# Performance work log

Hardware: AMD Instinct MI355X
Metric: run time of the kernel (lower is better)

## Reference

```python
import jax, jax.numpy as jnp
import numpy as np

RADIUS = 0.12
N_SAMPLE = 32


def ball_query(radius, n_sample, xyz, new_xyz):
    """Faithful replication of pointnet2 ball_query CUDA semantics.

    For each query point, take the FIRST n_sample points (in index order)
    with squared distance < radius^2. If fewer than n_sample are found,
    remaining slots repeat the first found index. If none found, idx = 0.
    """
    B, N, _ = xyz.shape
    # d2[b,p,n] = ||new_xyz[b,p] - xyz[b,n]||^2 via expansion (avoids [B,P,N,3])
    qq = jnp.sum(new_xyz * new_xyz, axis=-1)[:, :, None]          # [B,P,1]
    xx = jnp.sum(xyz * xyz, axis=-1)[:, None, :]                  # [B,1,N]
    qx = jnp.einsum('bpd,bnd->bpn', new_xyz, xyz)                 # [B,P,N]
    d2 = qq + xx - 2.0 * qx
    mask = d2 < radius * radius
    # score = N - n for in-ball points (strictly decreasing in n), 0 otherwise.
    # top_k then yields the first n_sample in-ball indices in ascending n order.
    score = jnp.where(mask, (N - jnp.arange(N, dtype=jnp.int32))[None, None, :],
                      jnp.int32(0))
    vals, idx = jax.lax.top_k(score, n_sample)                    # [B,P,S]
    valid = vals > 0
    first = jnp.where(valid[..., :1], idx[..., :1], 0)            # 0 if no neighbor
    return jnp.where(valid, idx, first).astype(jnp.int32)


def group(features, idx):
    """features: [B,C,N], idx: [B,P,S] -> [B,C,P,S]."""
    return jax.vmap(lambda f, i: f[:, i])(features, idx)


def setup_inputs() -> dict:
    key = jax.random.key(0)
    k1, k2, k3 = jax.random.split(key, 3)
    B, N, P, C = 4, 8192, 2048, 64
    xyz = jax.random.uniform(k1, (B, N, 3), dtype=jnp.float32)
    new_xyz = jax.random.uniform(k2, (B, P, 3), dtype=jnp.float32)
    features = jax.random.normal(k3, (B, C, N), dtype=jnp.float32)
    return {"xyz": xyz, "new_xyz": new_xyz, "features": features}


def reference(xyz, new_xyz, features):
    idx = ball_query(RADIUS, N_SAMPLE, xyz, new_xyz)              # [B,P,S] int32
    xyz_t = jnp.transpose(xyz, (0, 2, 1))                         # [B,3,N]
    grouped_xyz = group(xyz_t, idx)                               # [B,3,P,S]
    grouped_xyz = grouped_xyz - jnp.transpose(new_xyz, (0, 2, 1))[..., None]
    grouped_features = group(features, idx)                       # [B,C,P,S]
    return jnp.concatenate([grouped_xyz, grouped_features], axis=1)  # [B,3+C,P,S]
```

## Files before the change

### kernel.cpp

```cpp
#include <hip/hip_runtime.h>

constexpr int kB = 4;
constexpr int kN = 8192;
constexpr int kP = 2048;
constexpr int kS = 32;
constexpr int kC = 64;
constexpr int kCO = 67;
constexpr float kR2 = 0.0144f;

__device__ __forceinline__ float sq3(float x, float y, float z) {
  return __fadd_rn(__fadd_rn(__fmul_rn(x, x), __fmul_rn(y, y)),
                   __fmul_rn(z, z));
}
__device__ __forceinline__ float dot3(float ax, float ay, float az, float bx,
                                      float by, float bz) {
  return __fadd_rn(__fadd_rn(__fmul_rn(ax, bx), __fmul_rn(ay, by)),
                   __fmul_rn(az, bz));
}

__global__ __launch_bounds__(256) void bq_k3(const float* __restrict__ xyz,
                                             const float* __restrict__ new_xyz,
                                             int* __restrict__ g_idx) {
  __shared__ unsigned short sidx[4][32];
  __shared__ int scnt[4];

  const int tid = threadIdx.x;
  const int wv = tid >> 6;
  const int lane = tid & 63;
  const int q = blockIdx.x * 4 + wv;
  const int b = q >> 11;
  const int p = q & (kP - 1);

  const float* xb = xyz + (size_t)b * kN * 3;
  const float* qb = new_xyz + ((size_t)b * kP + p) * 3;

  const float qx = qb[0], qy = qb[1], qz = qb[2];
  const float qq = sq3(qx, qy, qz);

  const unsigned long long lmask = (1ull << lane) - 1ull;
  int cnt = 0;

  float cx[4], cy[4], cz[4];
#pragma unroll
  for (int k = 0; k < 4; ++k) {
    int n = k * 64 + lane;
    cx[k] = xb[3 * n + 0];
    cy[k] = xb[3 * n + 1];
    cz[k] = xb[3 * n + 2];
  }

  int gbase = 0;
  for (int g0 = 256;; g0 += 256) {
    const bool more = (g0 < kN);
    const int g1 = more ? g0 : 0;
    float nx[4], ny[4], nz[4];
#pragma unroll
    for (int k = 0; k < 4; ++k) {
      int n = g1 + k * 64 + lane;
      nx[k] = xb[3 * n + 0];
      ny[k] = xb[3 * n + 1];
      nz[k] = xb[3 * n + 2];
    }
#pragma unroll
    for (int k = 0; k < 4; ++k) {
      const float px = cx[k], py = cy[k], pz = cz[k];
      const float xx = sq3(px, py, pz);
      const int ncur = gbase + k * 64 + lane;
      float d2 = __fsub_rn(__fadd_rn(qq, xx),
                           __fmul_rn(2.0f, dot3(qx, qy, qz, px, py, pz)));
      unsigned long long m = __ballot(d2 < kR2);
      if (m) {
        int pos = cnt + __popcll(m & lmask);
        if ((d2 < kR2) && pos < kS)
          sidx[wv][pos] = (unsigned short)ncur;
        cnt += __popcll(m);
      }
    }
    if (!more || cnt >= kS) break;
#pragma unroll
    for (int k = 0; k < 4; ++k) {
      cx[k] = nx[k];
      cy[k] = ny[k];
      cz[k] = nz[k];
    }
    gbase = g0;
  }

  if (lane == 0) scnt[wv] = cnt;
  __syncthreads();

  if (lane < kS) {
    int c = scnt[wv];
    int first = (c > 0) ? (int)sidx[wv][0] : 0;
    int val = (lane < c) ? (int)sidx[wv][lane] : first;
    g_idx[((size_t)(b * kP + p)) * kS + lane] = val;
  }
}

__global__ __launch_bounds__(512) void gather_k2(
    const float* __restrict__ xyz, const float* __restrict__ new_xyz,
    const float* __restrict__ feat, const int* __restrict__ g_idx,
    float* __restrict__ out) {
  __shared__ float row[kN];
  __shared__ float nxz[kP / 2];
  const int tid = threadIdx.x;
  const int bi = blockIdx.x;
  const int b = bi / (kCO * 2);
  const int r = bi % (kCO * 2);
  const int c = r >> 1;
  const int ph = r & 1;

  if (c < 3) {
    for (int i = tid; i < kN; i += 512)
      row[i] = xyz[((size_t)b * kN + i) * 3 + c];
    for (int i = tid; i < kP / 2; i += 512)
      nxz[i] = new_xyz[((size_t)b * kP + ph * (kP / 2) + i) * 3 + c];
  } else {
    const float4* src = (const float4*)(feat + ((size_t)b * kC + (c - 3)) * kN);
    float4* dst = (float4*)row;
    for (int i = tid; i < kN / 4; i += 512) dst[i] = src[i];
  }
  __syncthreads();

  const size_t eg_base = (((size_t)b * kP + ph * (kP / 2)) * kS) >> 2;
  const int4* idx4 = (const int4*)g_idx + eg_base;
  float4* out4 =
      (float4*)out + ((((size_t)b * kCO + c) * kP + ph * (kP / 2)) * kS >> 2);
  const bool isxyz = (c < 3);
#pragma unroll 4
  for (int it = 0; it < (kP / 2) * kS / 4 / 512; ++it) {
    const int e4 = it * 512 + tid;
    const int4 n = idx4[e4];
    float4 v = make_float4(row[n.x], row[n.y], row[n.z], row[n.w]);
    if (isxyz) {
      const float sub = nxz[e4 >> 3];
      v.x = __fsub_rn(v.x, sub);
      v.y = __fsub_rn(v.y, sub);
      v.z = __fsub_rn(v.z, sub);
      v.w = __fsub_rn(v.w, sub);
    }
    out4[e4] = v;
  }
}

__global__ __launch_bounds__(512) void fused_qg(
    const float* __restrict__ xyz, const float* __restrict__ new_xyz,
    const float* __restrict__ feat, float* __restrict__ out) {
  __shared__ __align__(16) char ls[32768 + 512 + 4096];
  unsigned short (*sidx)[64][32] = (unsigned short (*)[64][32])ls;
  float* row = (float*)ls;
  unsigned char (*scnt)[64] = (unsigned char (*)[64])(ls + 32768);
  unsigned short (*midx)[32] = (unsigned short (*)[32])(ls + 32768 + 512);

  const int tid = threadIdx.x;
  const int wv = tid >> 6;
  const int lane = tid & 63;
  const int b = blockIdx.x >> 5;
  const int p0 = (blockIdx.x & 31) << 6;

  {
    const float* q = &new_xyz[(b * kP + p0 + lane) * 3];
    const float qx = q[0], qy = q[1], qz = q[2];
    const float qq = sq3(qx, qy, qz);
    const float* xb = xyz + ((size_t)b * kN + wv * 1024) * 3;
    int cnt = 0;
    for (int i = 0; i < 1024; ++i) {
      float px = xb[i * 3 + 0], py = xb[i * 3 + 1], pz = xb[i * 3 + 2];
      float xx = sq3(px, py, pz);
      float d2 = __fsub_rn(__fadd_rn(qq, xx),
                           __fmul_rn(2.0f, dot3(qx, qy, qz, px, py, pz)));
      if (d2 < kR2 && cnt < kS) {
        sidx[wv][lane][cnt] = (unsigned short)(wv * 1024 + i);
        ++cnt;
      }
    }
    scnt[wv][lane] = (unsigned char)cnt;
  }
  __syncthreads();

  if (tid < 64) {
    int filled = 0, first = 0;
    bool has = false;
    for (int sg = 0; sg < 8 && filled < kS; ++sg) {
      int c = scnt[sg][tid];
      for (int k = 0; k < c && filled < kS; ++k) {
        int n = sidx[sg][tid][k];
        if (!has) { first = n; has = true; }
        midx[tid][filled++] = (unsigned short)n;
      }
    }
    for (; filled < kS; ++filled) midx[tid][filled] = (unsigned short)first;
  }

  for (int c = 0; c < kCO; ++c) {
    __syncthreads();
    if (c < 3) {
      for (int i = tid; i < kN; i += 512)
        row[i] = xyz[((size_t)b * kN + i) * 3 + c];
    } else {
      const float4* src =
          (const float4*)(feat + ((size_t)b * kC + (c - 3)) * kN);
      float4* dst = (float4*)row;
      for (int i = tid; i < kN / 4; i += 512) dst[i] = src[i];
    }
    __syncthreads();
    const int outbase = ((b * kCO + c) * kP + p0) * kS;
    for (int e = tid; e < 64 * kS; e += 512) {
      int n = midx[e >> 5][e & 31];
      float v = row[n];
      if (c < 3) v = __fsub_rn(v, new_xyz[(b * kP + p0 + (e >> 5)) * 3 + c]);
      out[outbase + e] = v;
    }
  }
}

extern "C" void kernel_launch(void* const* d_in, const int* in_sizes, int n_in,
                              void* d_out, int out_size, void* d_ws,
                              size_t ws_size, hipStream_t stream) {
  const float* xyz = (const float*)d_in[0];
  const float* new_xyz = (const float*)d_in[1];
  const float* feat = (const float*)d_in[2];
  float* out = (float*)d_out;

  const size_t idx_bytes = (size_t)kB * kP * kS * sizeof(int);
  if (ws_size >= idx_bytes) {
    int* g_idx = (int*)d_ws;
    bq_k3<<<dim3(kB * kP / 4), dim3(256), 0, stream>>>(xyz, new_xyz, g_idx);
    gather_k2<<<dim3(kB * kCO * 2), dim3(512), 0, stream>>>(xyz, new_xyz, feat,
                                                            g_idx, out);
  } else {
    fused_qg<<<dim3(kB * (kP / 64)), dim3(512), 0, stream>>>(xyz, new_xyz,
                                                             feat, out);
  }
}
```

Measured before the change: 49.78 us.

## Replace linear ball-query scan with uniform-grid binning and neighbor-cell search

Adds a binning kernel that buckets each batch's points into an 8x8x8 uniform grid, with fixed capacity 64 per cell, using atomics. The count and slot buffers live in the output buffer as scratch, which the gather kernel overwrites afterwards. The ball query now tests only the 27 neighboring cells (cell size 0.125, larger than the 0.12 radius) instead of scanning points in index order until 32 hits are found. It then recovers index order with a wave-level bitonic sort or a repeated-min selection. This removes most distance tests, but adds a memset, an extra kernel launch and sorting work. Points beyond the per-cell cap are silently dropped, which could change results for dense inputs.

```diff
diff --git a/kernel.cpp b/kernel.cpp
--- a/kernel.cpp
+++ b/kernel.cpp
@@ -8,6 +8,10 @@
 constexpr int kCO = 67;
 constexpr float kR2 = 0.0144f;
 
+constexpr int kG = 8;
+constexpr int kCells = kG * kG * kG;
+constexpr int kCap = 64;
+
 __device__ __forceinline__ float sq3(float x, float y, float z) {
   return __fadd_rn(__fadd_rn(__fmul_rn(x, x), __fmul_rn(y, y)),
                    __fmul_rn(z, z));
@@ -18,11 +22,31 @@
                    __fmul_rn(az, bz));
 }
 
-__global__ __launch_bounds__(256) void bq_k3(const float* __restrict__ xyz,
-                                             const float* __restrict__ new_xyz,
-                                             int* __restrict__ g_idx) {
-  __shared__ unsigned short sidx[4][32];
-  __shared__ int scnt[4];
+__device__ __forceinline__ int cell_of(float x) {
+  int c = (int)(x * 8.0f);
+  return c > 7 ? 7 : (c < 0 ? 0 : c);
+}
+
+__global__ __launch_bounds__(256) void bin_k(const float* __restrict__ xyz,
+                                             int* __restrict__ cnt,
+                                             float4* __restrict__ slots) {
+  const int i = blockIdx.x * 256 + threadIdx.x;
+  const int b = i >> 13;
+  const int n = i & (kN - 1);
+  const float x = xyz[3 * i + 0];
+  const float y = xyz[3 * i + 1];
+  const float z = xyz[3 * i + 2];
+  const int gid =
+      b * kCells + (cell_of(z) * kG + cell_of(y)) * kG + cell_of(x);
+  const int pos = atomicAdd(&cnt[gid], 1);
+  if (pos < kCap)
+    slots[(size_t)gid * kCap + pos] = make_float4(x, y, z, __int_as_float(n));
+}
+
+__global__ __launch_bounds__(256) void bq_grid(
+    const float* __restrict__ new_xyz, const int* __restrict__ cnt,
+    const float4* __restrict__ slots, int* __restrict__ g_idx) {
+  __shared__ unsigned short plist[4][256];
 
   const int tid = threadIdx.x;
   const int wv = tid >> 6;
@@ -31,70 +55,96 @@
   const int b = q >> 11;
   const int p = q & (kP - 1);
 
-  const float* xb = xyz + (size_t)b * kN * 3;
   const float* qb = new_xyz + ((size_t)b * kP + p) * 3;
-
   const float qx = qb[0], qy = qb[1], qz = qb[2];
   const float qq = sq3(qx, qy, qz);
 
+  const int cqx = cell_of(qx), cqy = cell_of(qy), cqz = cell_of(qz);
+  const int x0 = cqx > 0 ? cqx - 1 : 0, x1 = cqx < 7 ? cqx + 1 : 7;
+  const int y0 = cqy > 0 ? cqy - 1 : 0, y1 = cqy < 7 ? cqy + 1 : 7;
+  const int z0 = cqz > 0 ? cqz - 1 : 0, z1 = cqz < 7 ? cqz + 1 : 7;
+
   const unsigned long long lmask = (1ull << lane) - 1ull;
-  int cnt = 0;
-
-  float cx[4], cy[4], cz[4];
+  int tp = 0;
+
+  for (int cz = z0; cz <= z1; ++cz)
+    for (int cy = y0; cy <= y1; ++cy)
+      for (int cx = x0; cx <= x1; ++cx) {
+        const int gid = b * kCells + (cz * kG + cy) * kG + cx;
+        int c = cnt[gid];
+        c = c > kCap ? kCap : c;
+        bool pass = false;
+        int idx = 0;
+        if (lane < c) {
+          const float4 s = slots[(size_t)gid * kCap + lane];
+          const float px = s.x, py = s.y, pz = s.z;
+          const float xx = sq3(px, py, pz);
+          const float d2 =
+              __fsub_rn(__fadd_rn(qq, xx),
+                        __fmul_rn(2.0f, dot3(qx, qy, qz, px, py, pz)));
+          pass = d2 < kR2;
+          idx = __float_as_int(s.w);
+        }
+        const unsigned long long m = __ballot(pass);
+        if (m) {
+          const int pos = tp + __popcll(m & lmask);
+          if (pass && pos < 256) plist[wv][pos] = (unsigned short)idx;
+          tp += __popcll(m);
+        }
+      }
+
+  int val;
+  if (tp <= 64) {
+    int v = (lane < tp) ? (int)plist[wv][lane] : 65535;
 #pragma unroll
-  for (int k = 0; k < 4; ++k) {
-    int n = k * 64 + lane;
-    cx[k] = xb[3 * n + 0];
-    cy[k] = xb[3 * n + 1];
-    cz[k] = xb[3 * n + 2];
-  }
-
-  int gbase = 0;
-  for (int g0 = 256;; g0 += 256) {
-    const bool more = (g0 < kN);
-    const int g1 = more ? g0 : 0;
-    float nx[4], ny[4], nz[4];
+    for (int k = 2; k <= 64; k <<= 1) {
 #pragma unroll
-    for (int k = 0; k < 4; ++k) {
-      int n = g1 + k * 64 + lane;
-      nx[k] = xb[3 * n + 0];
-      ny[k] = xb[3 * n + 1];
-      nz[k] = xb[3 * n + 2];
-    }
+      for (int j = k >> 1; j > 0; j >>= 1) {
+        const int pv = __shfl_xor(v, j);
+        const bool lower = (lane & j) == 0;
+        const bool asc = (lane & k) == 0;
+        v = (lower == asc) ? (v < pv ? v : pv) : (v > pv ? v : pv);
+      }
+    }
+    const int first = __shfl(v, 0);
+    val = (tp == 0) ? 0 : ((lane < tp) ? v : first);
+  } else {
+    const int ctp = tp > 256 ? 256 : tp;
+    int v0 = (lane < ctp) ? (int)plist[wv][lane] : 65535;
+    int v1 = (lane + 64 < ctp) ? (int)plist[wv][lane + 64] : 65535;
+    int v2 = (lane + 128 < ctp) ? (int)plist[wv][lane + 128] : 65535;
+    int v3 = (lane + 192 < ctp) ? (int)plist[wv][lane + 192] : 65535;
+    int t;
+#define CSWP(a, b) \
+  if (a > b) {     \
+    t = a;         \
+    a = b;         \
+    b = t;         \
+  }
+    CSWP(v0, v1) CSWP(v2, v3) CSWP(v0, v2) CSWP(v1, v3) CSWP(v1, v2)
+#undef CSWP
+    int res = 0;
+    for (int r = 0; r < 32; ++r) {
+      int g = v0;
 #pragma unroll
-    for (int k = 0; k < 4; ++k) {
-      const float px = cx[k], py = cy[k], pz = cz[k];
-      const float xx = sq3(px, py, pz);
-      const int ncur = gbase + k * 64 + lane;
-      float d2 = __fsub_rn(__fadd_rn(qq, xx),
-                           __fmul_rn(2.0f, dot3(qx, qy, qz, px, py, pz)));
-      unsigned long long m = __ballot(d2 < kR2);
-      if (m) {
-        int pos = cnt + __popcll(m & lmask);
-        if ((d2 < kR2) && pos < kS)
-          sidx[wv][pos] = (unsigned short)ncur;
-        cnt += __popcll(m);
-      }
-    }
-    if (!more || cnt >= kS) break;
-#pragma unroll
-    for (int k = 0; k < 4; ++k) {
-      cx[k] = nx[k];
-      cy[k] = ny[k];
-      cz[k] = nz[k];
-    }
-    gbase = g0;
-  }
-
-  if (lane == 0) scnt[wv] = cnt;
-  __syncthreads();
-
-  if (lane < kS) {
-    int c = scnt[wv];
-    int first = (c > 0) ? (int)sidx[wv][0] : 0;
-    int val = (lane < c) ? (int)sidx[wv][lane] : first;
-    g_idx[((size_t)(b * kP + p)) * kS + lane] = val;
-  }
+      for (int off = 32; off > 0; off >>= 1) {
+        const int og = __shfl_xor(g, off);
+        g = og < g ? og : g;
+      }
+      const unsigned long long mm = __ballot(v0 == g);
+      const int win = __ffsll(mm) - 1;
+      if (lane == win) {
+        v0 = v1;
+        v1 = v2;
+        v2 = v3;
+        v3 = 65535;
+      }
+      if (lane == r) res = g;
+    }
+    val = res;
+  }
+
+  if (lane < kS) g_idx[((size_t)(b * kP + p)) * kS + lane] = val;
 }
 
 __global__ __launch_bounds__(512) void gather_k2(
@@ -225,7 +275,12 @@
   const size_t idx_bytes = (size_t)kB * kP * kS * sizeof(int);
   if (ws_size >= idx_bytes) {
     int* g_idx = (int*)d_ws;
-    bq_k3<<<dim3(kB * kP / 4), dim3(256), 0, stream>>>(xyz, new_xyz, g_idx);
+    int* cnt = (int*)d_out;
+    float4* slots = (float4*)((char*)d_out + kB * kCells * sizeof(int));
+    hipMemsetAsync(cnt, 0, kB * kCells * sizeof(int), stream);
+    bin_k<<<dim3(kB * kN / 256), dim3(256), 0, stream>>>(xyz, cnt, slots);
+    bq_grid<<<dim3(kB * kP / 4), dim3(256), 0, stream>>>(new_xyz, cnt, slots,
+                                                         g_idx);
     gather_k2<<<dim3(kB * kCO * 2), dim3(512), 0, stream>>>(xyz, new_xyz, feat,
                                                             g_idx, out);
   } else {
```

After: 55.85 us. 1.12x slower.
